# Performance work log

Measured on AMD Instinct MI355X. Metric: run time of the kernel, lower is better.

Reference implementation:

```python
import jax, jax.numpy as jnp
import numpy as np

N, D, H, C = 16384, 2048, 512, 65
EPS_LOG = 1e-6   # matches torch log(p + 1e-6)
EPS_NORM = 1e-12 # matches F.normalize default eps


def setup_inputs() -> dict:
    key = jax.random.key(0)
    k0, k1, k2 = jax.random.split(key, 3)
    return {
        "feat": jax.random.normal(k0, (N, D), jnp.float32),
        "w1": jax.random.normal(k1, (D, H), jnp.float32) * (1.0 / np.sqrt(D)),
        "b1": jnp.zeros((H,), jnp.float32),
        "w2": jax.random.normal(k2, (H, C), jnp.float32) * (1.0 / np.sqrt(H)),
        "b2": jnp.zeros((C,), jnp.float32),
    }


def reference(feat, w1, b1, w2, b2):
    n, c = feat.shape[0], w2.shape[1]
    # fc1 -> relu -> dropout(p=0.5, training=True; fixed key for determinism) -> fc2
    h = jax.nn.relu(feat @ w1 + b1)
    keep = jax.random.bernoulli(jax.random.key(42), 0.5, h.shape)
    h = jnp.where(keep, h * 2.0, 0.0)
    logits = h @ w2 + b2

    logp = jax.nn.log_softmax(logits, axis=1)
    p = jnp.exp(logp)  # softmax_out

    entropy = -jnp.mean(jnp.sum(p * jnp.log(p + EPS_LOG), axis=1))
    mean_p = jnp.mean(p, axis=0)
    diversity = jnp.sum(mean_p * jnp.log(mean_p + EPS_LOG))

    # per-class centroids: one-pass segment reduce instead of python loop over classes
    pseudo_preds = jnp.argmax(p, axis=1)
    sums = jax.ops.segment_sum(feat, pseudo_preds, num_segments=c)          # [C, D]
    counts = jax.ops.segment_sum(jnp.ones((n,), feat.dtype), pseudo_preds, num_segments=c)
    means = sums / jnp.maximum(counts, 1.0)[:, None]
    norms = jnp.linalg.norm(means, axis=1, keepdims=True)
    centroids = jnp.where(counts[:, None] > 0, means / jnp.maximum(norms, EPS_NORM), 0.0)

    feat_n = feat / jnp.maximum(jnp.linalg.norm(feat, axis=1, keepdims=True), EPS_NORM)
    sim = feat_n @ centroids.T                                              # [N, C]
    pseudo_labels = jnp.argmax(sim, axis=1)

    ce = -jnp.mean(jnp.take_along_axis(logp, pseudo_labels[:, None], axis=1))
    loss = entropy + diversity + 0.3 * ce
    return loss
```

## Files before the change

kernel.cpp:

```cpp
#include <hip/hip_runtime.h>

typedef unsigned short us;
typedef unsigned int u32;
typedef __attribute__((ext_vector_type(8))) short short8;
typedef __attribute__((ext_vector_type(4))) float f32x4;

#define MFMA16(a, b, c) __builtin_amdgcn_mfma_f32_16x16x32_bf16((a), (b), (c), 0, 0, 0)

#define GLD16(lptr, gptr) __builtin_amdgcn_global_load_lds( \
    (__attribute__((address_space(1))) void*)(gptr), \
    (__attribute__((address_space(3))) void*)(lptr), 16, 0, 0)

__device__ inline us f2bf(float f) {
  u32 u = __float_as_uint(f);
  u32 r = (u + 0x7FFFu + ((u >> 16) & 1u)) >> 16;
  return (us)r;
}
__device__ inline float bf2f(us s) { return __uint_as_float((u32)s << 16); }
__device__ inline void splitbf(float x, us& hi, us& lo) {
  hi = f2bf(x);
  lo = f2bf(x - bf2f(hi));
}

__global__ void k_init(float* accs, int* cnt, int* cursor) {
  int t = threadIdx.x;
  if (t < 68) accs[t] = 0.f;
  if (t < 65) { cnt[t] = 0; cursor[t] = 0; }
}

#define TF_R(a) { x0 += x1; x1 = (x1 << (a)) | (x1 >> (32 - (a))); x1 ^= x0; }
__global__ void k_mask(u32* __restrict__ mask) {
  u32 t = blockIdx.x * 256u + threadIdx.x;
  const u32 K0 = 0u, K1 = 42u, K2 = 0x1BD11BDAu ^ 0u ^ 42u;
  u32 w0 = 0, w1 = 0;
  for (int i = 0; i < 32; ++i) {
    u32 x0 = t * 32u + (u32)i;
    u32 x1 = x0 + 4194304u;
    x0 += K0; x1 += K1;
    TF_R(13) TF_R(15) TF_R(26) TF_R(6)   x0 += K1; x1 += K2 + 1u;
    TF_R(17) TF_R(29) TF_R(16) TF_R(24)  x0 += K2; x1 += K0 + 2u;
    TF_R(13) TF_R(15) TF_R(26) TF_R(6)   x0 += K0; x1 += K1 + 3u;
    TF_R(17) TF_R(29) TF_R(16) TF_R(24)  x0 += K1; x1 += K2 + 4u;
    TF_R(13) TF_R(15) TF_R(26) TF_R(6)   x0 += K2; x1 += K0 + 5u;
    w0 |= (u32)((x0 >> 31) == 0u) << i;
    w1 |= (u32)((x1 >> 31) == 0u) << i;
  }
  mask[t] = w0;
  mask[t + 131072u] = w1;
}

__global__ void k_splitw1(const float* __restrict__ w1, us* __restrict__ th, us* __restrict__ tl) {
  __shared__ float tile[64][65];
  int k0 = blockIdx.x * 64, n0 = blockIdx.y * 64;
  int t = threadIdx.x;
  int cr = t >> 6, cc = t & 63;
  for (int i = 0; i < 16; ++i) {
    int r = i * 4 + cr;
    tile[r][cc] = w1[(size_t)(k0 + r) * 512 + n0 + cc];
  }
  __syncthreads();
  for (int i = 0; i < 16; ++i) {
    int n = i * 4 + cr;
    int k = cc;
    us hi, lo; splitbf(tile[k][n], hi, lo);
    size_t o = (size_t)(n0 + n) * 2048 + k0 + k;
    th[o] = hi; tl[o] = lo;
  }
}

__global__ void k_splitw2(const float* __restrict__ w2, us* __restrict__ th, us* __restrict__ tl) {
  int n = blockIdx.x;
  for (int k = threadIdx.x; k < 512; k += 256) {
    float v = (n < 65) ? w2[(size_t)k * 65 + n] : 0.f;
    us hi, lo; splitbf(v, hi, lo);
    th[n * 512 + k] = hi; tl[n * 512 + k] = lo;
  }
}

__global__ void k_splitfeat(const float* __restrict__ x, us* __restrict__ xh, us* __restrict__ xl) {
  size_t g = ((size_t)blockIdx.x * 256 + threadIdx.x) * 8;
  f32x4 a = *(const f32x4*)(x + g);
  f32x4 b = *(const f32x4*)(x + g + 4);
  short8 h8, l8;
  for (int i = 0; i < 4; ++i) {
    us hi, lo;
    splitbf(a[i], hi, lo); h8[i] = (short)hi; l8[i] = (short)lo;
    splitbf(b[i], hi, lo); h8[4 + i] = (short)hi; l8[4 + i] = (short)lo;
  }
  *(short8*)(xh + g) = h8;
  *(short8*)(xl + g) = l8;
}

__global__ __launch_bounds__(256, 2) void k_gemm1(
    const us* __restrict__ Ah_, const us* __restrict__ Al_,
    const us* __restrict__ Bh_, const us* __restrict__ Bl_,
    const float* __restrict__ b1, const u32* __restrict__ mask,
    us* __restrict__ Hh, us* __restrict__ Hl) {
  __shared__ __align__(16) us lds[4 * 4096];
  us* sAh = lds; us* sAl = lds + 4096; us* sBh = lds + 8192; us* sBl = lds + 12288;
  int tid = threadIdx.x;
  int bn = blockIdx.x, bm = blockIdx.y;
  int m0 = bm * 128, n0 = bn * 128;
  int lane = tid & 63, wv = tid >> 6;
  int wm = (wv >> 1) * 64, wn = (wv & 1) * 64;
  int frow = lane & 15, fk = (lane >> 4) * 8;
  int srow = tid >> 2, scol = (tid & 3) * 8;
  f32x4 acc[4][4] = {};
  size_t arow = (size_t)(m0 + srow) * 2048 + scol;
  size_t brow = (size_t)(n0 + srow) * 2048 + scol;
  for (int kt = 0; kt < 64; ++kt) {
    int k0 = kt * 32;
    __syncthreads();
    GLD16(sAh + wv * 512,        Ah_ + arow + k0);
    GLD16(sAh + 2048 + wv * 512, Ah_ + arow + (size_t)64 * 2048 + k0);
    GLD16(sAl + wv * 512,        Al_ + arow + k0);
    GLD16(sAl + 2048 + wv * 512, Al_ + arow + (size_t)64 * 2048 + k0);
    GLD16(sBh + wv * 512,        Bh_ + brow + k0);
    GLD16(sBh + 2048 + wv * 512, Bh_ + brow + (size_t)64 * 2048 + k0);
    GLD16(sBl + wv * 512,        Bl_ + brow + k0);
    GLD16(sBl + 2048 + wv * 512, Bl_ + brow + (size_t)64 * 2048 + k0);
    __syncthreads();
    short8 ah[4], al[4], bh[4], bl[4];
#pragma unroll
    for (int f = 0; f < 4; ++f) {
      ah[f] = *(const short8*)&sAh[(wm + f * 16 + frow) * 32 + fk];
      al[f] = *(const short8*)&sAl[(wm + f * 16 + frow) * 32 + fk];
      bh[f] = *(const short8*)&sBh[(wn + f * 16 + frow) * 32 + fk];
      bl[f] = *(const short8*)&sBl[(wn + f * 16 + frow) * 32 + fk];
    }
#pragma unroll
    for (int i = 0; i < 4; ++i)
#pragma unroll
      for (int j = 0; j < 4; ++j) {
        acc[i][j] = MFMA16(ah[i], bh[j], acc[i][j]);
        acc[i][j] = MFMA16(ah[i], bl[j], acc[i][j]);
        acc[i][j] = MFMA16(al[i], bh[j], acc[i][j]);
      }
  }
#pragma unroll
  for (int i = 0; i < 4; ++i)
#pragma unroll
    for (int j = 0; j < 4; ++j)
#pragma unroll
      for (int r = 0; r < 4; ++r) {
        int row = m0 + wm + i * 16 + (lane >> 4) * 4 + r;
        int col = n0 + wn + j * 16 + (lane & 15);
        float v = acc[i][j][r] + b1[col];
        v = fmaxf(v, 0.f);
        u32 f = (u32)row * 512u + (u32)col;
        u32 keep = (mask[f >> 5] >> (f & 31u)) & 1u;
        v = keep ? v * 2.f : 0.f;
        us hi, lo; splitbf(v, hi, lo);
        size_t o = (size_t)row * 512 + col;
        Hh[o] = hi; Hl[o] = lo;
      }
}

__global__ __launch_bounds__(256, 2) void k_gemm2(
    const us* __restrict__ Ah_, const us* __restrict__ Al_,
    const us* __restrict__ Bh_, const us* __restrict__ Bl_,
    const float* __restrict__ b2,
    float* __restrict__ logp, int* __restrict__ preds,
    float* __restrict__ accs ) {
  __shared__ __align__(16) us sA[2][2048];
  __shared__ __align__(16) us sB[2][2560];
  __shared__ float slog[64 * 81];
  __shared__ float sm[64], sl[64];
  __shared__ float sred[256];
  int tid = threadIdx.x;
  int m0 = blockIdx.x * 64;
  int lane = tid & 63, wv = tid >> 6;
  int frow = lane & 15, fk = (lane >> 4) * 8;
  int srow = tid >> 2, scol = (tid & 3) * 8;
  int r2 = 64 + (lane >> 2), sc2 = (lane & 3) * 8;
  f32x4 acc[5] = {};
  size_t arow = (size_t)(m0 + srow) * 512 + scol;
  size_t brow = (size_t)srow * 512 + scol;
  size_t brow2 = (size_t)r2 * 512 + sc2;
  for (int kt = 0; kt < 16; ++kt) {
    int k0 = kt * 32;
    __syncthreads();
    GLD16(&sA[0][wv * 512], Ah_ + arow + k0);
    GLD16(&sA[1][wv * 512], Al_ + arow + k0);
    GLD16(&sB[0][wv * 512], Bh_ + brow + k0);
    GLD16(&sB[1][wv * 512], Bl_ + brow + k0);
    if (wv == 0) {
      GLD16(&sB[0][2048], Bh_ + brow2 + k0);
      GLD16(&sB[1][2048], Bl_ + brow2 + k0);
    }
    __syncthreads();
    short8 a_h = *(const short8*)&sA[0][(wv * 16 + frow) * 32 + fk];
    short8 a_l = *(const short8*)&sA[1][(wv * 16 + frow) * 32 + fk];
#pragma unroll
    for (int fn = 0; fn < 5; ++fn) {
      short8 b_h = *(const short8*)&sB[0][(fn * 16 + frow) * 32 + fk];
      short8 b_l = *(const short8*)&sB[1][(fn * 16 + frow) * 32 + fk];
      acc[fn] = MFMA16(a_h, b_h, acc[fn]);
      acc[fn] = MFMA16(a_h, b_l, acc[fn]);
      acc[fn] = MFMA16(a_l, b_h, acc[fn]);
    }
  }
#pragma unroll
  for (int fn = 0; fn < 5; ++fn) {
    int col = fn * 16 + (lane & 15);
    if (col < 65) {
      float bb = b2[col];
#pragma unroll
      for (int r = 0; r < 4; ++r) {
        int row = wv * 16 + (lane >> 4) * 4 + r;
        slog[row * 81 + col] = acc[fn][r] + bb;
      }
    }
  }
  __syncthreads();
  if (tid < 64) {
    int row = tid;
    float m = -1e30f; int am = 0;
    for (int c = 0; c < 65; ++c) {
      float v = slog[row * 81 + c];
      if (v > m) { m = v; am = c; }
    }
    float s = 0.f;
    for (int c = 0; c < 65; ++c) s += expf(slog[row * 81 + c] - m);
    sm[row] = m; sl[row] = logf(s);
    preds[m0 + row] = am;
  }
  __syncthreads();
  float entp = 0.f;
  if (tid < 240) {
    int c = tid % 80, rr0 = tid / 80;
    if (c < 65) {
      float mpp = 0.f;
      for (int r = rr0; r < 64; r += 3) {
        float v = slog[r * 81 + c] - sm[r] - sl[r];
        logp[(size_t)(m0 + r) * 65 + c] = v;
        float p = expf(v);
        mpp += p;
        entp += p * logf(p + 1e-6f);
      }
      atomicAdd(&accs[2 + c], mpp);
    }
  }
  sred[tid] = entp;
  __syncthreads();
  for (int s = 128; s > 0; s >>= 1) { if (tid < s) sred[tid] += sred[tid + s]; __syncthreads(); }
  if (tid == 0) atomicAdd(&accs[0], sred[0]);
}

__global__ __launch_bounds__(256) void k_hist(const int* __restrict__ preds, int* __restrict__ cnt) {
  __shared__ int h[65];
  int tid = threadIdx.x;
  if (tid < 65) h[tid] = 0;
  __syncthreads();
  int i = blockIdx.x * 256 + tid;
  atomicAdd(&h[preds[i]], 1);
  __syncthreads();
  if (tid < 65 && h[tid] > 0) atomicAdd(&cnt[tid], h[tid]);
}

__global__ void k_scan(const int* __restrict__ cnt, int* __restrict__ base) {
  if (threadIdx.x == 0) {
    int s = 0;
    for (int c = 0; c < 65; ++c) { base[c] = s; s += cnt[c]; }
  }
}

__global__ __launch_bounds__(256) void k_scatter(
    const int* __restrict__ preds, const int* __restrict__ base,
    int* __restrict__ cursor, int* __restrict__ rowidx) {
  __shared__ int h[65];
  __shared__ int gb[65];
  int tid = threadIdx.x;
  if (tid < 65) h[tid] = 0;
  __syncthreads();
  int i = blockIdx.x * 256 + tid;
  int c = preds[i];
  int pos = atomicAdd(&h[c], 1);
  __syncthreads();
  if (tid < 65 && h[tid] > 0) gb[tid] = atomicAdd(&cursor[tid], h[tid]);
  __syncthreads();
  rowidx[base[c] + gb[c] + pos] = i;
}

__global__ __launch_bounds__(256) void k_segsum2(
    const float* __restrict__ feat, const int* __restrict__ rowidx,
    const int* __restrict__ base, const int* __restrict__ cnt,
    float* __restrict__ psum ) {
  int c = blockIdx.x;
  int j = blockIdx.y;
  int tid = threadIdx.x;
  int start = base[c], n = cnt[c];
  f32x4 a0 = {}, a1 = {};
  const float* fp = feat + (size_t)tid * 8;
  for (int i = j; i < n; i += 8) {
    int row = rowidx[start + i];
    const f32x4* p = (const f32x4*)(fp + (size_t)row * 2048);
    a0 += p[0];
    a1 += p[1];
  }
  float* o = psum + ((size_t)(j * 65 + c)) * 2048 + (size_t)tid * 8;
  *(f32x4*)o = a0;
  *(f32x4*)(o + 4) = a1;
}

__global__ __launch_bounds__(256) void k_centroid(
    const float* __restrict__ psum, const int* __restrict__ pcnt,
    us* __restrict__ ch, us* __restrict__ cl) {
  int c = blockIdx.x;
  int tid = threadIdx.x;
  if (c >= 65) {
    for (int d = tid; d < 2048; d += 256) { ch[(size_t)c * 2048 + d] = 0; cl[(size_t)c * 2048 + d] = 0; }
    return;
  }
  int cnt = pcnt[c];
  float inv = 1.0f / (float)((cnt > 1) ? cnt : 1);
  float mean[8]; float sq = 0.f;
  for (int i = 0; i < 8; ++i) {
    int d = tid + i * 256;
    float s = 0.f;
    for (int nc = 0; nc < 8; ++nc) s += psum[((size_t)nc * 65 + c) * 2048 + d];
    mean[i] = s * inv;
    sq += mean[i] * mean[i];
  }
  __shared__ float red[256];
  red[tid] = sq; __syncthreads();
  for (int s = 128; s > 0; s >>= 1) { if (tid < s) red[tid] += red[tid + s]; __syncthreads(); }
  float norm = sqrtf(red[0]);
  float dscale = (cnt > 0) ? 1.0f / fmaxf(norm, 1e-12f) : 0.0f;
  for (int i = 0; i < 8; ++i) {
    int d = tid + i * 256;
    us hi, lo; splitbf(mean[i] * dscale, hi, lo);
    ch[(size_t)c * 2048 + d] = hi; cl[(size_t)c * 2048 + d] = lo;
  }
}

__global__ __launch_bounds__(256, 2) void k_sim(
    const us* __restrict__ Ah_, const us* __restrict__ Al_,
    const us* __restrict__ Bh_, const us* __restrict__ Bl_,
    const float* __restrict__ logp, float* __restrict__ accs ) {
  __shared__ __align__(16) us sA[2][2048];
  __shared__ __align__(16) us sB[2][2560];
  __shared__ float ssim[64 * 81];
  __shared__ float sred[256];
  int tid = threadIdx.x;
  int m0 = blockIdx.x * 64;
  int lane = tid & 63, wv = tid >> 6;
  int frow = lane & 15, fk = (lane >> 4) * 8;
  int srow = tid >> 2, scol = (tid & 3) * 8;
  int r2 = 64 + (lane >> 2), sc2 = (lane & 3) * 8;
  f32x4 acc[5] = {};
  size_t arow = (size_t)(m0 + srow) * 2048 + scol;
  size_t brow = (size_t)srow * 2048 + scol;
  size_t brow2 = (size_t)r2 * 2048 + sc2;
  for (int kt = 0; kt < 64; ++kt) {
    int k0 = kt * 32;
    __syncthreads();
    GLD16(&sA[0][wv * 512], Ah_ + arow + k0);
    GLD16(&sA[1][wv * 512], Al_ + arow + k0);
    GLD16(&sB[0][wv * 512], Bh_ + brow + k0);
    GLD16(&sB[1][wv * 512], Bl_ + brow + k0);
    if (wv == 0) {
      GLD16(&sB[0][2048], Bh_ + brow2 + k0);
      GLD16(&sB[1][2048], Bl_ + brow2 + k0);
    }
    __syncthreads();
    short8 a_h = *(const short8*)&sA[0][(wv * 16 + frow) * 32 + fk];
    short8 a_l = *(const short8*)&sA[1][(wv * 16 + frow) * 32 + fk];
#pragma unroll
    for (int fn = 0; fn < 5; ++fn) {
      short8 b_h = *(const short8*)&sB[0][(fn * 16 + frow) * 32 + fk];
      short8 b_l = *(const short8*)&sB[1][(fn * 16 + frow) * 32 + fk];
      acc[fn] = MFMA16(a_h, b_h, acc[fn]);
      acc[fn] = MFMA16(a_h, b_l, acc[fn]);
      acc[fn] = MFMA16(a_l, b_h, acc[fn]);
    }
  }
#pragma unroll
  for (int fn = 0; fn < 5; ++fn) {
    int col = fn * 16 + (lane & 15);
    if (col < 65)
#pragma unroll
      for (int r = 0; r < 4; ++r)
        ssim[(wv * 16 + (lane >> 4) * 4 + r) * 81 + col] = acc[fn][r];
  }
  __syncthreads();
  float cep = 0.f;
  if (tid < 64) {
    float m = -1e30f; int am = 0;
    for (int c = 0; c < 65; ++c) {
      float v = ssim[tid * 81 + c];
      if (v > m) { m = v; am = c; }
    }
    cep = logp[(size_t)(m0 + tid) * 65 + am];
  }
  sred[tid] = cep;
  __syncthreads();
  for (int s = 128; s > 0; s >>= 1) { if (tid < s) sred[tid] += sred[tid + s]; __syncthreads(); }
  if (tid == 0) atomicAdd(&accs[1], sred[0]);
}

__global__ void k_final(const float* __restrict__ accs, float* __restrict__ out) {
  __shared__ float red[256];
  int t = threadIdx.x;
  float d = 0.f;
  if (t < 65) {
    float mp = accs[2 + t] * (1.f / 16384.f);
    d = mp * logf(mp + 1e-6f);
  }
  red[t] = d; __syncthreads();
  for (int s = 128; s > 0; s >>= 1) { if (t < s) red[t] += red[t + s]; __syncthreads(); }
  if (t == 0) {
    float entropy = -accs[0] * (1.f / 16384.f);
    float ce = -accs[1] * (1.f / 16384.f);
    out[0] = entropy + red[0] + 0.3f * ce;
  }
}

extern "C" void kernel_launch(void* const* d_in, const int* in_sizes, int n_in,
                              void* d_out, int out_size, void* d_ws, size_t ws_size,
                              hipStream_t stream) {
  const float* feat = (const float*)d_in[0];
  const float* w1   = (const float*)d_in[1];
  const float* b1   = (const float*)d_in[2];
  const float* w2   = (const float*)d_in[3];
  const float* b2   = (const float*)d_in[4];
  float* out = (float*)d_out;

  char* w = (char*)d_ws;
  auto alloc = [&](size_t b) { char* p = w; w += (b + 255) & ~(size_t)255; return p; };
  us*  feat_hi = (us*)alloc(16384ull * 2048 * 2);
  us*  feat_lo = (us*)alloc(16384ull * 2048 * 2);
  us*  w1t_hi  = (us*)alloc(512ull * 2048 * 2);
  us*  w1t_lo  = (us*)alloc(512ull * 2048 * 2);
  us*  w2t_hi  = (us*)alloc(80ull * 512 * 2);
  us*  w2t_lo  = (us*)alloc(80ull * 512 * 2);
  u32* mask    = (u32*)alloc(262144ull * 4);
  us*  h_hi    = (us*)alloc(16384ull * 512 * 2);
  us*  h_lo    = (us*)alloc(16384ull * 512 * 2);
  float* logp  = (float*)alloc(16384ull * 65 * 4);
  int*   preds = (int*)alloc(16384ull * 4);
  float* psum  = (float*)alloc(8ull * 65 * 2048 * 4);
  int*   cnt   = (int*)alloc(65ull * 4);
  int*   base  = (int*)alloc(65ull * 4);
  int*   cursor= (int*)alloc(65ull * 4);
  int*   rowidx= (int*)alloc(16384ull * 4);
  us*  cent_hi = (us*)alloc(80ull * 2048 * 2);
  us*  cent_lo = (us*)alloc(80ull * 2048 * 2);
  float* accs  = (float*)alloc(68ull * 4);

  k_init<<<1, 256, 0, stream>>>(accs, cnt, cursor);
  k_mask<<<512, 256, 0, stream>>>(mask);
  k_splitw1<<<dim3(32, 8), 256, 0, stream>>>(w1, w1t_hi, w1t_lo);
  k_splitw2<<<80, 256, 0, stream>>>(w2, w2t_hi, w2t_lo);
  k_splitfeat<<<16384, 256, 0, stream>>>(feat, feat_hi, feat_lo);
  k_gemm1<<<dim3(4, 128), 256, 0, stream>>>(feat_hi, feat_lo, w1t_hi, w1t_lo, b1, mask, h_hi, h_lo);
  k_gemm2<<<256, 256, 0, stream>>>(h_hi, h_lo, w2t_hi, w2t_lo, b2, logp, preds, accs);
  k_hist<<<64, 256, 0, stream>>>(preds, cnt);
  k_scan<<<1, 64, 0, stream>>>(cnt, base);
  k_scatter<<<64, 256, 0, stream>>>(preds, base, cursor, rowidx);
  k_segsum2<<<dim3(65, 8), 256, 0, stream>>>(feat, rowidx, base, cnt, psum);
  k_centroid<<<80, 256, 0, stream>>>(psum, cnt, cent_hi, cent_lo);
  k_sim<<<256, 256, 0, stream>>>(feat_hi, feat_lo, cent_hi, cent_lo, logp, accs);
  k_final<<<1, 256, 0, stream>>>(accs, out);
}
```

Measured before the change: 560.3 us.

## Double K tile with XOR-swizzled LDS, reorder gemm1 grid, split-K the sim GEMM

All three GEMMs now use a K step of 64 instead of 32, which halves the number of barrier-separated iterations. LDS rows are XOR-swizzled to avoid bank conflicts on the wider rows. The gemm1 grid is transposed so neighbouring blocks share the same W1 column tile. The similarity GEMM is split along K into two halves across a second grid dimension, writing partial sums to a new buffer that a new reduction kernel adds up before the argmax and CE sum. This raises parallelism for the 256-block kernel but adds an extra launch and global traffic, and doubles LDS per block, which may reduce occupancy.

```diff
diff --git a/kernel.cpp b/kernel.cpp
--- a/kernel.cpp
+++ b/kernel.cpp
@@ -96,46 +96,54 @@
     const us* __restrict__ Bh_, const us* __restrict__ Bl_,
     const float* __restrict__ b1, const u32* __restrict__ mask,
     us* __restrict__ Hh, us* __restrict__ Hl) {
-  __shared__ __align__(16) us lds[4 * 4096];
-  us* sAh = lds; us* sAl = lds + 4096; us* sBh = lds + 8192; us* sBl = lds + 12288;
-  int tid = threadIdx.x;
-  int bn = blockIdx.x, bm = blockIdx.y;
+  __shared__ __align__(16) us lds[4 * 8192];
+  us* sAh = lds; us* sAl = lds + 8192; us* sBh = lds + 16384; us* sBl = lds + 24576;
+  int tid = threadIdx.x;
+  int bm = blockIdx.x, bn = blockIdx.y;
   int m0 = bm * 128, n0 = bn * 128;
   int lane = tid & 63, wv = tid >> 6;
   int wm = (wv >> 1) * 64, wn = (wv & 1) * 64;
-  int frow = lane & 15, fk = (lane >> 4) * 8;
-  int srow = tid >> 2, scol = (tid & 3) * 8;
+  int frow = lane & 15, fq = lane >> 4;
+  int srow = tid >> 3;
+  int scolsw = (((tid & 7) ^ ((tid >> 3) & 7)) * 8);
   f32x4 acc[4][4] = {};
-  size_t arow = (size_t)(m0 + srow) * 2048 + scol;
-  size_t brow = (size_t)(n0 + srow) * 2048 + scol;
-  for (int kt = 0; kt < 64; ++kt) {
-    int k0 = kt * 32;
-    __syncthreads();
-    GLD16(sAh + wv * 512,        Ah_ + arow + k0);
-    GLD16(sAh + 2048 + wv * 512, Ah_ + arow + (size_t)64 * 2048 + k0);
-    GLD16(sAl + wv * 512,        Al_ + arow + k0);
-    GLD16(sAl + 2048 + wv * 512, Al_ + arow + (size_t)64 * 2048 + k0);
-    GLD16(sBh + wv * 512,        Bh_ + brow + k0);
-    GLD16(sBh + 2048 + wv * 512, Bh_ + brow + (size_t)64 * 2048 + k0);
-    GLD16(sBl + wv * 512,        Bl_ + brow + k0);
-    GLD16(sBl + 2048 + wv * 512, Bl_ + brow + (size_t)64 * 2048 + k0);
-    __syncthreads();
-    short8 ah[4], al[4], bh[4], bl[4];
-#pragma unroll
-    for (int f = 0; f < 4; ++f) {
-      ah[f] = *(const short8*)&sAh[(wm + f * 16 + frow) * 32 + fk];
-      al[f] = *(const short8*)&sAl[(wm + f * 16 + frow) * 32 + fk];
-      bh[f] = *(const short8*)&sBh[(wn + f * 16 + frow) * 32 + fk];
-      bl[f] = *(const short8*)&sBl[(wn + f * 16 + frow) * 32 + fk];
-    }
-#pragma unroll
-    for (int i = 0; i < 4; ++i)
-#pragma unroll
-      for (int j = 0; j < 4; ++j) {
-        acc[i][j] = MFMA16(ah[i], bh[j], acc[i][j]);
-        acc[i][j] = MFMA16(ah[i], bl[j], acc[i][j]);
-        acc[i][j] = MFMA16(al[i], bh[j], acc[i][j]);
-      }
+  size_t arow = (size_t)(m0 + srow) * 2048 + scolsw;
+  size_t brow = (size_t)(n0 + srow) * 2048 + scolsw;
+  for (int kt = 0; kt < 32; ++kt) {
+    int k0 = kt * 64;
+    __syncthreads();
+#pragma unroll
+    for (int j = 0; j < 4; ++j) {
+      int lo = j * 2048 + wv * 512;
+      size_t go = (size_t)j * 32 * 2048 + k0;
+      GLD16(sAh + lo, Ah_ + arow + go);
+      GLD16(sAl + lo, Al_ + arow + go);
+      GLD16(sBh + lo, Bh_ + brow + go);
+      GLD16(sBl + lo, Bl_ + brow + go);
+    }
+    __syncthreads();
+#pragma unroll
+    for (int s = 0; s < 2; ++s) {
+      short8 ah[4], al[4], bh[4], bl[4];
+#pragma unroll
+      for (int f = 0; f < 4; ++f) {
+        int ca = ((s * 4 + fq) ^ (frow & 7)) * 8;
+        int ra = (wm + f * 16 + frow) * 64 + ca;
+        int rb = (wn + f * 16 + frow) * 64 + ca;
+        ah[f] = *(const short8*)&sAh[ra];
+        al[f] = *(const short8*)&sAl[ra];
+        bh[f] = *(const short8*)&sBh[rb];
+        bl[f] = *(const short8*)&sBl[rb];
+      }
+#pragma unroll
+      for (int i = 0; i < 4; ++i)
+#pragma unroll
+        for (int j2 = 0; j2 < 4; ++j2) {
+          acc[i][j2] = MFMA16(ah[i], bh[j2], acc[i][j2]);
+          acc[i][j2] = MFMA16(ah[i], bl[j2], acc[i][j2]);
+          acc[i][j2] = MFMA16(al[i], bh[j2], acc[i][j2]);
+        }
+    }
   }
 #pragma unroll
   for (int i = 0; i < 4; ++i)
@@ -162,42 +170,51 @@
     const float* __restrict__ b2,
     float* __restrict__ logp, int* __restrict__ preds,
     float* __restrict__ accs ) {
-  __shared__ __align__(16) us sA[2][2048];
-  __shared__ __align__(16) us sB[2][2560];
+  __shared__ __align__(16) us sA[2][4096];
+  __shared__ __align__(16) us sB[2][5120];
   __shared__ float slog[64 * 81];
   __shared__ float sm[64], sl[64];
   __shared__ float sred[256];
   int tid = threadIdx.x;
   int m0 = blockIdx.x * 64;
   int lane = tid & 63, wv = tid >> 6;
-  int frow = lane & 15, fk = (lane >> 4) * 8;
-  int srow = tid >> 2, scol = (tid & 3) * 8;
-  int r2 = 64 + (lane >> 2), sc2 = (lane & 3) * 8;
+  int frow = lane & 15, fq = lane >> 4;
+  int srow = tid >> 3;
+  int scolsw = (((tid & 7) ^ ((tid >> 3) & 7)) * 8);
   f32x4 acc[5] = {};
-  size_t arow = (size_t)(m0 + srow) * 512 + scol;
-  size_t brow = (size_t)srow * 512 + scol;
-  size_t brow2 = (size_t)r2 * 512 + sc2;
-  for (int kt = 0; kt < 16; ++kt) {
-    int k0 = kt * 32;
-    __syncthreads();
-    GLD16(&sA[0][wv * 512], Ah_ + arow + k0);
-    GLD16(&sA[1][wv * 512], Al_ + arow + k0);
-    GLD16(&sB[0][wv * 512], Bh_ + brow + k0);
-    GLD16(&sB[1][wv * 512], Bl_ + brow + k0);
-    if (wv == 0) {
-      GLD16(&sB[0][2048], Bh_ + brow2 + k0);
-      GLD16(&sB[1][2048], Bl_ + brow2 + k0);
-    }
-    __syncthreads();
-    short8 a_h = *(const short8*)&sA[0][(wv * 16 + frow) * 32 + fk];
-    short8 a_l = *(const short8*)&sA[1][(wv * 16 + frow) * 32 + fk];
-#pragma unroll
-    for (int fn = 0; fn < 5; ++fn) {
-      short8 b_h = *(const short8*)&sB[0][(fn * 16 + frow) * 32 + fk];
-      short8 b_l = *(const short8*)&sB[1][(fn * 16 + frow) * 32 + fk];
-      acc[fn] = MFMA16(a_h, b_h, acc[fn]);
-      acc[fn] = MFMA16(a_h, b_l, acc[fn]);
-      acc[fn] = MFMA16(a_l, b_h, acc[fn]);
+  size_t arow = (size_t)(m0 + srow) * 512 + scolsw;
+  size_t brow = (size_t)srow * 512 + scolsw;
+  size_t brow2 = (size_t)(64 + (tid >> 3)) * 512 + scolsw;
+  for (int kt = 0; kt < 8; ++kt) {
+    int k0 = kt * 64;
+    __syncthreads();
+#pragma unroll
+    for (int j = 0; j < 2; ++j) {
+      int lo = j * 2048 + wv * 512;
+      size_t go = (size_t)j * 32 * 512 + k0;
+      GLD16(&sA[0][lo], Ah_ + arow + go);
+      GLD16(&sA[1][lo], Al_ + arow + go);
+      GLD16(&sB[0][lo], Bh_ + brow + go);
+      GLD16(&sB[1][lo], Bl_ + brow + go);
+    }
+    if (wv < 2) {
+      GLD16(&sB[0][4096 + wv * 512], Bh_ + brow2 + k0);
+      GLD16(&sB[1][4096 + wv * 512], Bl_ + brow2 + k0);
+    }
+    __syncthreads();
+#pragma unroll
+    for (int s = 0; s < 2; ++s) {
+      int ca = ((s * 4 + fq) ^ (frow & 7)) * 8;
+      short8 a_h = *(const short8*)&sA[0][(wv * 16 + frow) * 64 + ca];
+      short8 a_l = *(const short8*)&sA[1][(wv * 16 + frow) * 64 + ca];
+#pragma unroll
+      for (int fn = 0; fn < 5; ++fn) {
+        short8 b_h = *(const short8*)&sB[0][(fn * 16 + frow) * 64 + ca];
+        short8 b_l = *(const short8*)&sB[1][(fn * 16 + frow) * 64 + ca];
+        acc[fn] = MFMA16(a_h, b_h, acc[fn]);
+        acc[fn] = MFMA16(a_h, b_l, acc[fn]);
+        acc[fn] = MFMA16(a_l, b_h, acc[fn]);
+      }
     }
   }
 #pragma unroll
@@ -337,63 +354,78 @@
 __global__ __launch_bounds__(256, 2) void k_sim(
     const us* __restrict__ Ah_, const us* __restrict__ Al_,
     const us* __restrict__ Bh_, const us* __restrict__ Bl_,
-    const float* __restrict__ logp, float* __restrict__ accs ) {
-  __shared__ __align__(16) us sA[2][2048];
-  __shared__ __align__(16) us sB[2][2560];
-  __shared__ float ssim[64 * 81];
-  __shared__ float sred[256];
+    float* __restrict__ simbuf ) {
+  __shared__ __align__(16) us sA[2][4096];
+  __shared__ __align__(16) us sB[2][5120];
   int tid = threadIdx.x;
   int m0 = blockIdx.x * 64;
+  int ks = blockIdx.y;
+  int kbase = ks * 1024;
   int lane = tid & 63, wv = tid >> 6;
-  int frow = lane & 15, fk = (lane >> 4) * 8;
-  int srow = tid >> 2, scol = (tid & 3) * 8;
-  int r2 = 64 + (lane >> 2), sc2 = (lane & 3) * 8;
+  int frow = lane & 15, fq = lane >> 4;
+  int srow = tid >> 3;
+  int scolsw = (((tid & 7) ^ ((tid >> 3) & 7)) * 8);
   f32x4 acc[5] = {};
-  size_t arow = (size_t)(m0 + srow) * 2048 + scol;
-  size_t brow = (size_t)srow * 2048 + scol;
-  size_t brow2 = (size_t)r2 * 2048 + sc2;
-  for (int kt = 0; kt < 64; ++kt) {
-    int k0 = kt * 32;
-    __syncthreads();
-    GLD16(&sA[0][wv * 512], Ah_ + arow + k0);
-    GLD16(&sA[1][wv * 512], Al_ + arow + k0);
-    GLD16(&sB[0][wv * 512], Bh_ + brow + k0);
-    GLD16(&sB[1][wv * 512], Bl_ + brow + k0);
-    if (wv == 0) {
-      GLD16(&sB[0][2048], Bh_ + brow2 + k0);
-      GLD16(&sB[1][2048], Bl_ + brow2 + k0);
-    }
-    __syncthreads();
-    short8 a_h = *(const short8*)&sA[0][(wv * 16 + frow) * 32 + fk];
-    short8 a_l = *(const short8*)&sA[1][(wv * 16 + frow) * 32 + fk];
-#pragma unroll
-    for (int fn = 0; fn < 5; ++fn) {
-      short8 b_h = *(const short8*)&sB[0][(fn * 16 + frow) * 32 + fk];
-      short8 b_l = *(const short8*)&sB[1][(fn * 16 + frow) * 32 + fk];
-      acc[fn] = MFMA16(a_h, b_h, acc[fn]);
-      acc[fn] = MFMA16(a_h, b_l, acc[fn]);
-      acc[fn] = MFMA16(a_l, b_h, acc[fn]);
+  size_t arow = (size_t)(m0 + srow) * 2048 + kbase + scolsw;
+  size_t brow = (size_t)srow * 2048 + kbase + scolsw;
+  size_t brow2 = (size_t)(64 + (tid >> 3)) * 2048 + kbase + scolsw;
+  for (int kt = 0; kt < 16; ++kt) {
+    int k0 = kt * 64;
+    __syncthreads();
+#pragma unroll
+    for (int j = 0; j < 2; ++j) {
+      int lo = j * 2048 + wv * 512;
+      size_t go = (size_t)j * 32 * 2048 + k0;
+      GLD16(&sA[0][lo], Ah_ + arow + go);
+      GLD16(&sA[1][lo], Al_ + arow + go);
+      GLD16(&sB[0][lo], Bh_ + brow + go);
+      GLD16(&sB[1][lo], Bl_ + brow + go);
+    }
+    if (wv < 2) {
+      GLD16(&sB[0][4096 + wv * 512], Bh_ + brow2 + k0);
+      GLD16(&sB[1][4096 + wv * 512], Bl_ + brow2 + k0);
+    }
+    __syncthreads();
+#pragma unroll
+    for (int s = 0; s < 2; ++s) {
+      int ca = ((s * 4 + fq) ^ (frow & 7)) * 8;
+      short8 a_h = *(const short8*)&sA[0][(wv * 16 + frow) * 64 + ca];
+      short8 a_l = *(const short8*)&sA[1][(wv * 16 + frow) * 64 + ca];
+#pragma unroll
+      for (int fn = 0; fn < 5; ++fn) {
+        short8 b_h = *(const short8*)&sB[0][(fn * 16 + frow) * 64 + ca];
+        short8 b_l = *(const short8*)&sB[1][(fn * 16 + frow) * 64 + ca];
+        acc[fn] = MFMA16(a_h, b_h, acc[fn]);
+        acc[fn] = MFMA16(a_h, b_l, acc[fn]);
+        acc[fn] = MFMA16(a_l, b_h, acc[fn]);
+      }
     }
   }
 #pragma unroll
   for (int fn = 0; fn < 5; ++fn) {
     int col = fn * 16 + (lane & 15);
-    if (col < 65)
-#pragma unroll
-      for (int r = 0; r < 4; ++r)
-        ssim[(wv * 16 + (lane >> 4) * 4 + r) * 81 + col] = acc[fn][r];
-  }
-  __syncthreads();
-  float cep = 0.f;
-  if (tid < 64) {
-    float m = -1e30f; int am = 0;
-    for (int c = 0; c < 65; ++c) {
-      float v = ssim[tid * 81 + c];
-      if (v > m) { m = v; am = c; }
-    }
-    cep = logp[(size_t)(m0 + tid) * 65 + am];
-  }
-  sred[tid] = cep;
+#pragma unroll
+    for (int r = 0; r < 4; ++r) {
+      int row = wv * 16 + (lane >> 4) * 4 + r;
+      simbuf[((size_t)(ks * 16384 + m0 + row)) * 80 + col] = acc[fn][r];
+    }
+  }
+}
+
+__global__ __launch_bounds__(256) void k_simred(
+    const float* __restrict__ simbuf, const float* __restrict__ logp,
+    float* __restrict__ accs ) {
+  __shared__ float sred[256];
+  int tid = threadIdx.x;
+  int row = blockIdx.x * 256 + tid;
+  const float* p0 = simbuf + (size_t)row * 80;
+  const float* p1 = simbuf + (size_t)(16384 + row) * 80;
+  float m = -1e30f; int am = 0;
+  for (int c = 0; c < 65; ++c) {
+    float v = p0[c] + p1[c];
+    if (v > m) { m = v; am = c; }
+  }
+  sred[tid] = logp[(size_t)row * 65 + am];
   __syncthreads();
   for (int s = 128; s > 0; s >>= 1) { if (tid < s) sred[tid] += sred[tid + s]; __syncthreads(); }
   if (tid == 0) atomicAdd(&accs[1], sred[0]);
@@ -446,6 +478,7 @@
   int*   rowidx= (int*)alloc(16384ull * 4);
   us*  cent_hi = (us*)alloc(80ull * 2048 * 2);
   us*  cent_lo = (us*)alloc(80ull * 2048 * 2);
+  float* simbuf= (float*)alloc(2ull * 16384 * 80 * 4);
   float* accs  = (float*)alloc(68ull * 4);
 
   k_init<<<1, 256, 0, stream>>>(accs, cnt, cursor);
@@ -453,13 +486,14 @@
   k_splitw1<<<dim3(32, 8), 256, 0, stream>>>(w1, w1t_hi, w1t_lo);
   k_splitw2<<<80, 256, 0, stream>>>(w2, w2t_hi, w2t_lo);
   k_splitfeat<<<16384, 256, 0, stream>>>(feat, feat_hi, feat_lo);
-  k_gemm1<<<dim3(4, 128), 256, 0, stream>>>(feat_hi, feat_lo, w1t_hi, w1t_lo, b1, mask, h_hi, h_lo);
+  k_gemm1<<<dim3(128, 4), 256, 0, stream>>>(feat_hi, feat_lo, w1t_hi, w1t_lo, b1, mask, h_hi, h_lo);
   k_gemm2<<<256, 256, 0, stream>>>(h_hi, h_lo, w2t_hi, w2t_lo, b2, logp, preds, accs);
   k_hist<<<64, 256, 0, stream>>>(preds, cnt);
   k_scan<<<1, 64, 0, stream>>>(cnt, base);
   k_scatter<<<64, 256, 0, stream>>>(preds, base, cursor, rowidx);
   k_segsum2<<<dim3(65, 8), 256, 0, stream>>>(feat, rowidx, base, cnt, psum);
   k_centroid<<<80, 256, 0, stream>>>(psum, cnt, cent_hi, cent_lo);
-  k_sim<<<256, 256, 0, stream>>>(feat_hi, feat_lo, cent_hi, cent_lo, logp, accs);
+  k_sim<<<dim3(256, 2), 256, 0, stream>>>(feat_hi, feat_lo, cent_hi, cent_lo, simbuf);
+  k_simred<<<64, 256, 0, stream>>>(simbuf, logp, accs);
   k_final<<<1, 256, 0, stream>>>(accs, out);
 }
```

Measured after the change: 534.6 us. -4.6%, faster.
